# Performance work log

Hardware: AMD Instinct MI355X
Metric: run time of the kernel (lower is better)

Reference implementation:

```python
import jax, jax.numpy as jnp
import numpy as np

EPS = 1e-10
LN_EPS = 1e-5
NEG = -1e30
H = 8  # attention_head


def _layernorm(x, g, b):
    mu = jnp.mean(x, axis=-1, keepdims=True)
    var = jnp.mean(jnp.square(x - mu), axis=-1, keepdims=True)
    return (x - mu) * jax.lax.rsqrt(var + LN_EPS) * g + b


def setup_inputs() -> dict:
    key = jax.random.key(0)
    ks = jax.random.split(key, 10)
    B, T, D = 4, 1024, 1024
    inputs = jax.random.normal(ks[0], (B, T, D), dtype=jnp.float32)
    lengths = jax.random.randint(ks[1], (B,), T // 2, T + 1).astype(jnp.int32)
    lengths = lengths.at[0].set(T)  # at least one full-length sequence
    noise_u = jax.random.uniform(ks[2], (B, H, T, T), dtype=jnp.float32)
    w = lambda k: (jax.random.normal(k, (D, D), dtype=jnp.float32) * 0.02)
    return {
        'inputs': inputs, 'lengths': lengths, 'noise_u': noise_u,
        'Wq': w(ks[3]), 'Wk': w(ks[4]), 'Wv': w(ks[5]),
        'Weq': w(ks[6]), 'Wek': w(ks[7]), 'Wfc': w(ks[8]),
        'bfc': jnp.zeros((D,), jnp.float32),
        'ln1_g': jnp.ones((D,), jnp.float32), 'ln1_b': jnp.zeros((D,), jnp.float32),
        'ln2_g': jnp.ones((D,), jnp.float32), 'ln2_b': jnp.zeros((D,), jnp.float32),
    }


def reference(inputs, lengths, noise_u, Wq, Wk, Wv, Weq, Wek, Wfc, bfc,
              ln1_g, ln1_b, ln2_g, ln2_b):
    B, T, D = inputs.shape
    dh = D // H
    # length mask: True where padded
    pad = jnp.arange(T)[None, :] >= lengths[:, None]            # (B, T)
    x = jnp.where(pad[:, :, None], 0.0, inputs)                  # zero padded positions

    def heads(W):
        h = x @ W.T                                              # (B,T,D)
        return h.reshape(B, T, H, dh).transpose(0, 2, 1, 3)      # (B,H,T,dh)

    q, k, v, eq, ek = (heads(W) for W in (Wq, Wk, Wv, Weq, Wek))
    scores = jnp.einsum('bhqd,bhkd->bhqk', q, k) / jnp.sqrt(jnp.float32(D))
    edge = jnp.einsum('bhqd,bhkd->bhqk', eq, ek)                 # (B,H,T,T)

    # bernoulli prior: binary-concrete sample (hard threshold), tau=1
    edges_prob = jax.nn.sigmoid(edge)
    logistic = jnp.log(noise_u + EPS) - jnp.log(1.0 - noise_u + EPS)
    y_soft = jax.nn.sigmoid(jnp.log(edges_prob + EPS) - jnp.log(1.0 - edges_prob + EPS) + logistic)
    gate = y_soft > 0.5                                          # hard edges (condition only, as in torch .data)

    valid = gate & (~pad[:, None, None, :])                      # gate AND key-length mask
    s = jnp.where(valid, scores, NEG)
    attn = jax.nn.softmax(s, axis=-1)
    attn = jnp.where(jnp.any(valid, axis=-1, keepdims=True), attn, 0.0)  # nan->0 for fully-masked rows

    ctx = jax.nn.relu(jnp.einsum('bhqk,bhkd->bhqd', attn, v))
    ctx = ctx.transpose(0, 2, 1, 3).reshape(B, T, D)

    h1 = _layernorm(ctx + x, ln1_g, ln1_b)
    h2 = jax.nn.relu(h1 @ Wfc.T + bfc) + h1
    out = _layernorm(h2, ln2_g, ln2_b)
    out = jnp.where(pad[:, :, None], 0.0, out)
    return out, attn, edges_prob
```

## Files before the change

kernel.cpp:

```cpp
#include <hip/hip_runtime.h>
#include <math.h>

constexpr int Bn = 4, Tn = 1024, Dn = 1024, Hn = 8, DH = 128;
constexpr float EPSF = 1e-10f;
constexpr float LN_EPSF = 1e-5f;
constexpr float NEGF = -1e30f;

typedef __attribute__((ext_vector_type(8))) short bf16x8;
typedef __attribute__((ext_vector_type(4))) float f32x4;
typedef __attribute__((ext_vector_type(4))) unsigned uint4v;

#define MFMA16(a, b, c) __builtin_amdgcn_mfma_f32_16x16x32_bf16(a, b, c, 0, 0, 0)

__device__ __forceinline__ short f2bf(float f) {
    unsigned u = __builtin_bit_cast(unsigned, f);
    u += 0x7fffu + ((u >> 16) & 1u);
    return (short)(u >> 16);
}
__device__ __forceinline__ float bf2f(short h) {
    return __builtin_bit_cast(float, ((unsigned)(unsigned short)h) << 16);
}
__device__ __forceinline__ unsigned pack2(float a, float b) {
    return ((unsigned)(unsigned short)f2bf(a)) | (((unsigned)(unsigned short)f2bf(b)) << 16);
}

__device__ __forceinline__ void gload16(const void* g, void* l) {
    __builtin_amdgcn_global_load_lds((__attribute__((address_space(1))) void*)g,
                                     (__attribute__((address_space(3))) void*)l,
                                     16, 0, 0);
}

template <int NW>
__device__ __forceinline__ void stage_b(const short* g, int ld, short* lds, int lane, int wid) {
#pragma unroll
    for (int s = 0; s < 8 / NW; ++s) {
        const int ii = wid * (8 / NW) + s;
        const int c = ii * 64 + lane;
        const int kb = c >> 7, r = c & 127;
        gload16(g + (size_t)r * ld + kb * 8, lds + ii * 512);
    }
}

template <int NT>
__device__ __forceinline__ void stage64(const short* g, int ld, short* lds, int lane, int wid) {
    constexpr int IT = 1024 / NT;
#pragma unroll
    for (int s = 0; s < IT; ++s) {
        const int cb = wid * IT + s;
        const int c = cb * 64 + lane;
        const int kb = c >> 7, r = c & 127;
        gload16(g + (size_t)r * ld + kb * 8, lds + cb * 512);
    }
}

template <int NW>
__device__ __forceinline__ void stage_f(const float* g, int ld, float* lds, int lane, int wid) {
#pragma unroll
    for (int s = 0; s < 16 / NW; ++s) {
        const int ii = wid * (16 / NW) + s;
        const int c = ii * 64 + lane;
        const int kb = c >> 8, half = (c >> 7) & 1, r = c & 127;
        gload16(g + (size_t)r * ld + kb * 8 + half * 4, lds + ii * 256);
    }
}

__device__ __forceinline__ bf16x8 fragb(const short* lds, int kbl, int r) {
    return *reinterpret_cast<const bf16x8*>(lds + kbl * 1024 + r * 8);
}

__device__ __forceinline__ bf16x8 fragf(const float* lds, int kbl, int r) {
    const f32x4 lo = *reinterpret_cast<const f32x4*>(lds + kbl * 1024 + r * 4);
    const f32x4 hi = *reinterpret_cast<const f32x4*>(lds + kbl * 1024 + 512 + r * 4);
    uint4v p;
    p[0] = pack2(lo[0], lo[1]);
    p[1] = pack2(lo[2], lo[3]);
    p[2] = pack2(hi[0], hi[1]);
    p[3] = pack2(hi[2], hi[3]);
    return __builtin_bit_cast(bf16x8, p);
}

struct CvtP { const float* src[6]; short* hi; short* lo; };

__global__ __launch_bounds__(256) void cvt_w(CvtP p) {
    const int i = blockIdx.x * 256 + threadIdx.x;
    const int mat = i >> 17;
    const int off = (i & 131071) * 8;
    const float* s = p.src[mat] + off;
    const float4 a = *reinterpret_cast<const float4*>(s);
    const float4 b = *reinterpret_cast<const float4*>(s + 4);
    const float va[8] = {a.x, a.y, a.z, a.w, b.x, b.y, b.z, b.w};
    bf16x8 h, l;
#pragma unroll
    for (int j = 0; j < 8; ++j) {
        h[j] = f2bf(va[j]);
        l[j] = f2bf(va[j] - bf2f(h[j]));
    }
    *reinterpret_cast<bf16x8*>(p.hi + (size_t)mat * 1048576 + off) = h;
    if (mat == 3 || mat == 4)
        *reinterpret_cast<bf16x8*>(p.lo + (size_t)(mat - 3) * 1048576 + off) = l;
}

__global__ __launch_bounds__(256) void mask_x(const float4* __restrict__ in,
                                              const int* __restrict__ lengths,
                                              short* __restrict__ xhi,
                                              short* __restrict__ xlo) {
    const int i = blockIdx.x * 256 + threadIdx.x;
    const int row = i >> 8;
    const int t = row & 1023, b = row >> 10;
    float4 v = in[i];
    if (t >= lengths[b]) { v.x = 0.f; v.y = 0.f; v.z = 0.f; v.w = 0.f; }
    short4 h, l;
    h.x = f2bf(v.x); h.y = f2bf(v.y); h.z = f2bf(v.z); h.w = f2bf(v.w);
    l.x = f2bf(v.x - bf2f(h.x)); l.y = f2bf(v.y - bf2f(h.y));
    l.z = f2bf(v.z - bf2f(h.z)); l.w = f2bf(v.w - bf2f(h.w));
    *reinterpret_cast<short4*>(xhi + (size_t)i * 4) = h;
    *reinterpret_cast<short4*>(xlo + (size_t)i * 4) = l;
}

struct Proj3P { const short* w[3]; short* o[3]; };

__global__ __launch_bounds__(256) void proj3_mfma(const short* __restrict__ Xh, Proj3P p) {
    __shared__ alignas(16) short T0[8192];
    __shared__ alignas(16) short T1[8192];
    const int z = blockIdx.z;
    const short* __restrict__ Wh = p.w[z];
    const int m0 = blockIdx.y << 7, n0 = blockIdx.x << 7;
    const int tid = threadIdx.x, lane = tid & 63, wid = tid >> 6;
    const int wm = (wid >> 1) << 6, wn = (wid & 1) << 6;
    const int kbl = lane >> 4, rl = lane & 15, rw = (lane >> 4) << 2;
    f32x4 acc[4][4] = {};
    for (int k0 = 0; k0 < Dn; k0 += 64) {
        stage64<256>(Xh + (size_t)m0 * Dn + k0, Dn, T0, lane, wid);
        stage64<256>(Wh + (size_t)n0 * Dn + k0, Dn, T1, lane, wid);
        __syncthreads();
#pragma unroll
        for (int hh = 0; hh < 2; ++hh) {
            bf16x8 a[4], b[4];
#pragma unroll
            for (int f = 0; f < 4; ++f) {
                a[f] = fragb(T0, hh * 4 + kbl, wm + f * 16 + rl);
                b[f] = fragb(T1, hh * 4 + kbl, wn + f * 16 + rl);
            }
#pragma unroll
            for (int i = 0; i < 4; ++i)
#pragma unroll
                for (int j = 0; j < 4; ++j)
                    acc[i][j] = MFMA16(a[i], b[j], acc[i][j]);
        }
        __syncthreads();
    }
    short* __restrict__ O = p.o[z];
#pragma unroll
    for (int i = 0; i < 4; ++i)
#pragma unroll
        for (int r = 0; r < 4; ++r) {
            const int m = m0 + wm + i * 16 + rw + r;
            const int b = m >> 10, t = m & 1023;
#pragma unroll
            for (int j = 0; j < 4; ++j) {
                const int n = n0 + wn + j * 16 + rl;
                const int h = n >> 7, d = n & 127;
                const short val = f2bf(acc[i][j][r]);
                if (z == 2)
                    O[(((size_t)(b * Hn + h) * DH + d) << 10) + t] = val;
                else
                    O[((((size_t)(b * Hn + h)) << 10) + t) * DH + d] = val;
            }
        }
}

struct Proj2P { const short* wh[2]; const short* wl[2]; short* oh[2]; short* ol[2]; };

__global__ __launch_bounds__(512) void proj2_mfma(const short* __restrict__ Xh,
                                                  const short* __restrict__ Xl, Proj2P p) {
    __shared__ alignas(16) short T0[8192];
    __shared__ alignas(16) short T1[8192];
    __shared__ alignas(16) short T2[8192];
    __shared__ alignas(16) short T3[8192];
    const int z = blockIdx.z;
    const short* __restrict__ Wh = p.wh[z];
    const short* __restrict__ Wl = p.wl[z];
    const int m0 = blockIdx.y << 7, n0 = blockIdx.x << 7;
    const int tid = threadIdx.x, lane = tid & 63, wid = tid >> 6;
    const int wm = (wid >> 2) << 6, wn = (wid & 3) << 5;
    const int kbl = lane >> 4, rl = lane & 15, rw = (lane >> 4) << 2;
    f32x4 acc[4][2] = {};
    for (int k0 = 0; k0 < Dn; k0 += 64) {
        stage64<512>(Xh + (size_t)m0 * Dn + k0, Dn, T0, lane, wid);
        stage64<512>(Xl + (size_t)m0 * Dn + k0, Dn, T1, lane, wid);
        stage64<512>(Wh + (size_t)n0 * Dn + k0, Dn, T2, lane, wid);
        stage64<512>(Wl + (size_t)n0 * Dn + k0, Dn, T3, lane, wid);
        __syncthreads();
#pragma unroll
        for (int hh = 0; hh < 2; ++hh) {
            bf16x8 ah[4], al[4], bh[2], bl[2];
#pragma unroll
            for (int f = 0; f < 4; ++f) {
                ah[f] = fragb(T0, hh * 4 + kbl, wm + f * 16 + rl);
                al[f] = fragb(T1, hh * 4 + kbl, wm + f * 16 + rl);
            }
#pragma unroll
            for (int f = 0; f < 2; ++f) {
                bh[f] = fragb(T2, hh * 4 + kbl, wn + f * 16 + rl);
                bl[f] = fragb(T3, hh * 4 + kbl, wn + f * 16 + rl);
            }
#pragma unroll
            for (int i = 0; i < 4; ++i)
#pragma unroll
                for (int j = 0; j < 2; ++j) {
                    acc[i][j] = MFMA16(al[i], bh[j], acc[i][j]);
                    acc[i][j] = MFMA16(ah[i], bl[j], acc[i][j]);
                    acc[i][j] = MFMA16(ah[i], bh[j], acc[i][j]);
                }
        }
        __syncthreads();
    }
    short* __restrict__ OH = p.oh[z];
    short* __restrict__ OL = p.ol[z];
#pragma unroll
    for (int i = 0; i < 4; ++i)
#pragma unroll
        for (int r = 0; r < 4; ++r) {
            const int m = m0 + wm + i * 16 + rw + r;
            const int b = m >> 10, t = m & 1023;
#pragma unroll
            for (int j = 0; j < 2; ++j) {
                const int n = n0 + wn + j * 16 + rl;
                const int h = n >> 7, d = n & 127;
                const size_t idx = (((size_t)(b * Hn + h)) << 10 | t) * DH + d;
                const float av = acc[i][j][r];
                const short hi = f2bf(av);
                OH[idx] = hi;
                OL[idx] = f2bf(av - bf2f(hi));
            }
        }
}

__global__ __launch_bounds__(256) void scores_edge(
    const short* __restrict__ Q, const short* __restrict__ Kb,
    const short* __restrict__ EQh, const short* __restrict__ EQl,
    const short* __restrict__ EKh, const short* __restrict__ EKl,
    const float* __restrict__ U, const int* __restrict__ lens,
    float* __restrict__ S, float* __restrict__ EP,
    float* __restrict__ Sm, float* __restrict__ Sl) {
    __shared__ alignas(16) short T0[4096];
    __shared__ alignas(16) short T1[4096];
    __shared__ alignas(16) short T2[4096];
    __shared__ alignas(16) short T3[4096];
    const int z = blockIdx.z;
    const int len = lens[z >> 3];
    const int m0 = blockIdx.y << 7, n0 = blockIdx.x << 7;
    const int tid = threadIdx.x, lane = tid & 63, wid = tid >> 6;
    const int wm = (wid >> 1) << 6, wn = (wid & 1) << 6;
    const int kbl = lane >> 4, rl = lane & 15, rw = (lane >> 4) << 2;
    const size_t zo = (size_t)z << 17;

    f32x4 acce[4][4] = {};
    for (int k0 = 0; k0 < DH; k0 += 32) {
        stage_b<4>(EQh + zo + (size_t)m0 * DH + k0, DH, T0, lane, wid);
        stage_b<4>(EQl + zo + (size_t)m0 * DH + k0, DH, T1, lane, wid);
        stage_b<4>(EKh + zo + (size_t)n0 * DH + k0, DH, T2, lane, wid);
        stage_b<4>(EKl + zo + (size_t)n0 * DH + k0, DH, T3, lane, wid);
        __syncthreads();
        bf16x8 ah[4], al[4], bh[4], bl[4];
#pragma unroll
        for (int f = 0; f < 4; ++f) {
            ah[f] = fragb(T0, kbl, wm + f * 16 + rl);
            al[f] = fragb(T1, kbl, wm + f * 16 + rl);
            bh[f] = fragb(T2, kbl, wn + f * 16 + rl);
            bl[f] = fragb(T3, kbl, wn + f * 16 + rl);
        }
#pragma unroll
        for (int i = 0; i < 4; ++i)
#pragma unroll
            for (int j = 0; j < 4; ++j) {
                acce[i][j] = MFMA16(al[i], bh[j], acce[i][j]);
                acce[i][j] = MFMA16(ah[i], bl[j], acce[i][j]);
                acce[i][j] = MFMA16(ah[i], bh[j], acce[i][j]);
            }
        __syncthreads();
    }

    f32x4 accs[4][4] = {};
    for (int k0 = 0; k0 < DH; k0 += 32) {
        stage_b<4>(Q + zo + (size_t)m0 * DH + k0, DH, T0, lane, wid);
        stage_b<4>(Kb + zo + (size_t)n0 * DH + k0, DH, T1, lane, wid);
        __syncthreads();
        bf16x8 a[4], b[4];
#pragma unroll
        for (int f = 0; f < 4; ++f) {
            a[f] = fragb(T0, kbl, wm + f * 16 + rl);
            b[f] = fragb(T1, kbl, wn + f * 16 + rl);
        }
#pragma unroll
        for (int i = 0; i < 4; ++i)
#pragma unroll
            for (int j = 0; j < 4; ++j)
                accs[i][j] = MFMA16(a[i], b[j], accs[i][j]);
        __syncthreads();
    }

    const size_t part = ((size_t)(z * 16 + blockIdx.x * 2 + (wn >> 6)) << 10);
#pragma unroll
    for (int i = 0; i < 4; ++i)
#pragma unroll
        for (int r = 0; r < 4; ++r) {
            const int m = m0 + wm + i * 16 + rw + r;
            float sv[4];
#pragma unroll
            for (int j = 0; j < 4; ++j) {
                const int n = n0 + wn + j * 16 + rl;
                const size_t idx = ((size_t)z << 20) + ((size_t)m << 10) + n;
                const float e = acce[i][j][r];
                EP[idx] = 1.f / (1.f + __expf(-e));
                const float u = U[idx];
                const float zz = e + __logf(u + EPSF) - __logf(1.f - u + EPSF);
                const bool valid = (zz > 0.f) && (n < len);
                const float s_val = valid ? accs[i][j][r] * (1.f / 32.f) : NEGF;
                S[idx] = s_val;
                sv[j] = s_val;
            }
            float mx = fmaxf(fmaxf(sv[0], sv[1]), fmaxf(sv[2], sv[3]));
#pragma unroll
            for (int off = 1; off <= 8; off <<= 1) mx = fmaxf(mx, __shfl_xor(mx, off));
            float ls = __expf(sv[0] - mx) + __expf(sv[1] - mx) +
                       __expf(sv[2] - mx) + __expf(sv[3] - mx);
#pragma unroll
            for (int off = 1; off <= 8; off <<= 1) ls += __shfl_xor(ls, off);
            if (rl == 0) { Sm[part + m] = mx; Sl[part + m] = ls; }
        }
}

__global__ __launch_bounds__(512) void softmax_ctx(float* __restrict__ P,
                                                   const float* __restrict__ Sm,
                                                   const float* __restrict__ Sl,
                                                   const short* __restrict__ Vt,
                                                   float* __restrict__ C) {
    __shared__ alignas(16) float Ps[4096];
    __shared__ alignas(16) short Vs[4096];
    const int z = blockIdx.y;
    const int bb = z >> 3, h = z & 7;
    const int m0 = blockIdx.x << 7;
    const int tid = threadIdx.x, lane = tid & 63, wid = tid >> 6;

    {
        const int r = tid >> 2, qd = tid & 3;
        const int row = m0 + r;
        float M = -3.0e38f;
#pragma unroll
        for (int t = 0; t < 16; ++t) M = fmaxf(M, Sm[((size_t)(z * 16 + t) << 10) + row]);
        float L = 0.f;
#pragma unroll
        for (int t = 0; t < 16; ++t)
            L += Sl[((size_t)(z * 16 + t) << 10) + row] *
                 __expf(Sm[((size_t)(z * 16 + t) << 10) + row] - M);
        const float inv = (M > -5e29f) ? 1.f / L : 0.f;
        float* rowp = P + ((size_t)z << 20) + ((size_t)row << 10) + qd * 8;
#pragma unroll 8
        for (int c = 0; c < 32; ++c) {
            float4 v0 = *reinterpret_cast<const float4*>(rowp + c * 32);
            float4 v1 = *reinterpret_cast<const float4*>(rowp + c * 32 + 4);
            v0.x = __expf(v0.x - M) * inv; v0.y = __expf(v0.y - M) * inv;
            v0.z = __expf(v0.z - M) * inv; v0.w = __expf(v0.w - M) * inv;
            v1.x = __expf(v1.x - M) * inv; v1.y = __expf(v1.y - M) * inv;
            v1.z = __expf(v1.z - M) * inv; v1.w = __expf(v1.w - M) * inv;
            *reinterpret_cast<float4*>(rowp + c * 32) = v0;
            *reinterpret_cast<float4*>(rowp + c * 32 + 4) = v1;
        }
    }
    __syncthreads();

    const int wm = (wid >> 2) << 6, wn = (wid & 3) << 5;
    const int kbl = lane >> 4, rl = lane & 15, rw = (lane >> 4) << 2;
    f32x4 acc[4][2] = {};
    for (int k0 = 0; k0 < Tn; k0 += 32) {
        stage_f<8>(P + ((size_t)z << 20) + ((size_t)m0 << 10) + k0, Tn, Ps, lane, wid);
        stage_b<8>(Vt + ((size_t)z << 17) + k0, Tn, Vs, lane, wid);
        __syncthreads();
        bf16x8 a[4], b[2];
#pragma unroll
        for (int f = 0; f < 4; ++f) a[f] = fragf(Ps, kbl, wm + f * 16 + rl);
#pragma unroll
        for (int f = 0; f < 2; ++f) b[f] = fragb(Vs, kbl, wn + f * 16 + rl);
#pragma unroll
        for (int i = 0; i < 4; ++i)
#pragma unroll
            for (int j = 0; j < 2; ++j)
                acc[i][j] = MFMA16(a[i], b[j], acc[i][j]);
        __syncthreads();
    }
#pragma unroll
    for (int i = 0; i < 4; ++i)
#pragma unroll
        for (int r = 0; r < 4; ++r) {
            const int m = m0 + wm + i * 16 + rw + r;
#pragma unroll
            for (int j = 0; j < 2; ++j) {
                const int n = wn + j * 16 + rl;
                C[(((size_t)(bb << 10 | m)) << 10) + h * DH + n] = fmaxf(acc[i][j][r], 0.f);
            }
        }
}

__global__ __launch_bounds__(256) void ln1_kernel(const float* __restrict__ ctx,
                                                  const float* __restrict__ inputs,
                                                  const int* __restrict__ lengths,
                                                  const float* __restrict__ g,
                                                  const float* __restrict__ bb,
                                                  float* __restrict__ h1f,
                                                  short* __restrict__ h1hi) {
    __shared__ float red1[4];
    __shared__ float red2[4];
    const int row = blockIdx.x;
    const int t = row & 1023, b = row >> 10;
    const bool live = t < lengths[b];
    const size_t base = (size_t)row * Dn;
    const int tid = threadIdx.x;
    float4 v = reinterpret_cast<const float4*>(ctx + base)[tid];
    if (live) {
        const float4 r = reinterpret_cast<const float4*>(inputs + base)[tid];
        v.x += r.x; v.y += r.y; v.z += r.z; v.w += r.w;
    }
    float s = v.x + v.y + v.z + v.w;
#pragma unroll
    for (int off = 32; off >= 1; off >>= 1) s += __shfl_xor(s, off);
    if ((tid & 63) == 0) red1[tid >> 6] = s;
    __syncthreads();
    const float mu = (red1[0] + red1[1] + red1[2] + red1[3]) * (1.f / Dn);
    const float d0 = v.x - mu, d1 = v.y - mu, d2 = v.z - mu, d3 = v.w - mu;
    float sq = d0 * d0 + d1 * d1 + d2 * d2 + d3 * d3;
#pragma unroll
    for (int off = 32; off >= 1; off >>= 1) sq += __shfl_xor(sq, off);
    if ((tid & 63) == 0) red2[tid >> 6] = sq;
    __syncthreads();
    const float var = (red2[0] + red2[1] + red2[2] + red2[3]) * (1.f / Dn);
    const float rstd = rsqrtf(var + LN_EPSF);
    const float4 gv = reinterpret_cast<const float4*>(g)[tid];
    const float4 bv = reinterpret_cast<const float4*>(bb)[tid];
    float4 ov;
    ov.x = d0 * rstd * gv.x + bv.x;
    ov.y = d1 * rstd * gv.y + bv.y;
    ov.z = d2 * rstd * gv.z + bv.z;
    ov.w = d3 * rstd * gv.w + bv.w;
    reinterpret_cast<float4*>(h1f + base)[tid] = ov;
    short4 hs;
    hs.x = f2bf(ov.x); hs.y = f2bf(ov.y); hs.z = f2bf(ov.z); hs.w = f2bf(ov.w);
    reinterpret_cast<short4*>(h1hi + base)[tid] = hs;
}

__global__ __launch_bounds__(256) void fc_mfma(const short* __restrict__ Xh,
                                               const short* __restrict__ Wh,
                                               const float* __restrict__ bias,
                                               const float* __restrict__ H1f,
                                               float* __restrict__ O) {
    __shared__ alignas(16) short T0[8192];
    __shared__ alignas(16) short T1[8192];
    const int m0 = blockIdx.y << 7, n0 = blockIdx.x << 7;
    const int tid = threadIdx.x, lane = tid & 63, wid = tid >> 6;
    const int wm = (wid >> 1) << 6, wn = (wid & 1) << 6;
    const int kbl = lane >> 4, rl = lane & 15, rw = (lane >> 4) << 2;
    f32x4 acc[4][4] = {};
    for (int k0 = 0; k0 < Dn; k0 += 64) {
        stage64<256>(Xh + (size_t)m0 * Dn + k0, Dn, T0, lane, wid);
        stage64<256>(Wh + (size_t)n0 * Dn + k0, Dn, T1, lane, wid);
        __syncthreads();
#pragma unroll
        for (int hh = 0; hh < 2; ++hh) {
            bf16x8 a[4], b[4];
#pragma unroll
            for (int f = 0; f < 4; ++f) {
                a[f] = fragb(T0, hh * 4 + kbl, wm + f * 16 + rl);
                b[f] = fragb(T1, hh * 4 + kbl, wn + f * 16 + rl);
            }
#pragma unroll
            for (int i = 0; i < 4; ++i)
#pragma unroll
                for (int j = 0; j < 4; ++j)
                    acc[i][j] = MFMA16(a[i], b[j], acc[i][j]);
        }
        __syncthreads();
    }
#pragma unroll
    for (int i = 0; i < 4; ++i)
#pragma unroll
        for (int r = 0; r < 4; ++r) {
            const int m = m0 + wm + i * 16 + rw + r;
#pragma unroll
            for (int j = 0; j < 4; ++j) {
                const int n = n0 + wn + j * 16 + rl;
                const size_t idx = ((size_t)m << 10) + n;
                O[idx] = fmaxf(acc[i][j][r] + bias[n], 0.f) + H1f[idx];
            }
        }
}

__global__ __launch_bounds__(256) void ln2_kernel(const float* __restrict__ a,
                                                  const float* __restrict__ g,
                                                  const float* __restrict__ bb,
                                                  const int* __restrict__ lengths,
                                                  float* __restrict__ o) {
    __shared__ float red1[4];
    __shared__ float red2[4];
    const int row = blockIdx.x;
    const size_t base = (size_t)row * Dn;
    const int tid = threadIdx.x;
    float4 v = reinterpret_cast<const float4*>(a + base)[tid];
    float s = v.x + v.y + v.z + v.w;
#pragma unroll
    for (int off = 32; off >= 1; off >>= 1) s += __shfl_xor(s, off);
    if ((tid & 63) == 0) red1[tid >> 6] = s;
    __syncthreads();
    const float mu = (red1[0] + red1[1] + red1[2] + red1[3]) * (1.f / Dn);
    const float d0 = v.x - mu, d1 = v.y - mu, d2 = v.z - mu, d3 = v.w - mu;
    float sq = d0 * d0 + d1 * d1 + d2 * d2 + d3 * d3;
#pragma unroll
    for (int off = 32; off >= 1; off >>= 1) sq += __shfl_xor(sq, off);
    if ((tid & 63) == 0) red2[tid >> 6] = sq;
    __syncthreads();
    const float var = (red2[0] + red2[1] + red2[2] + red2[3]) * (1.f / Dn);
    const float rstd = rsqrtf(var + LN_EPSF);
    const float4 gv = reinterpret_cast<const float4*>(g)[tid];
    const float4 bv = reinterpret_cast<const float4*>(bb)[tid];
    float4 ov;
    ov.x = d0 * rstd * gv.x + bv.x;
    ov.y = d1 * rstd * gv.y + bv.y;
    ov.z = d2 * rstd * gv.z + bv.z;
    ov.w = d3 * rstd * gv.w + bv.w;
    const int t = row & 1023, b = row >> 10;
    if (t >= lengths[b]) { ov.x = 0.f; ov.y = 0.f; ov.z = 0.f; ov.w = 0.f; }
    reinterpret_cast<float4*>(o + base)[tid] = ov;
}

extern "C" void kernel_launch(void* const* d_in, const int* in_sizes, int n_in,
                              void* d_out, int out_size, void* d_ws, size_t ws_size,
                              hipStream_t stream) {
    const float* inputs = (const float*)d_in[0];
    const int* lengths = (const int*)d_in[1];
    const float* noise = (const float*)d_in[2];
    const float* bfc = (const float*)d_in[9];
    const float* ln1_g = (const float*)d_in[10];
    const float* ln1_b = (const float*)d_in[11];
    const float* ln2_g = (const float*)d_in[12];
    const float* ln2_b = (const float*)d_in[13];

    float* out = (float*)d_out;
    float* attn = out + (size_t)Bn * Tn * Dn;
    float* ep = attn + (size_t)Bn * Hn * Tn * Tn;

    constexpr size_t MB = 1u << 20;
    char* W = (char*)d_ws;
    short* xhi = (short*)(W + 0 * MB);
    short* xlo = (short*)(W + 8 * MB);
    short* whi = (short*)(W + 16 * MB);
    short* wlo = (short*)(W + 28 * MB);
    short* qb = (short*)(W + 34 * MB);
    short* kb = (short*)(W + 42 * MB);
    short* vtb = (short*)(W + 50 * MB);
    short* eqh = (short*)(W + 58 * MB);
    short* eql = (short*)(W + 66 * MB);
    short* ekh = (short*)(W + 74 * MB);
    short* ekl = (short*)(W + 82 * MB);
    float* ctx = (float*)(W + 58 * MB);
    float* h1f = (float*)(W + 74 * MB);
    short* h1hi = (short*)(W + 34 * MB);
    float* h2 = (float*)(W + 0 * MB);
    float* Sm = (float*)(W + 90 * MB);
    float* Sl = (float*)(W + 92 * MB);

    CvtP cp;
    for (int j = 0; j < 6; ++j) cp.src[j] = (const float*)d_in[3 + j];
    cp.hi = whi; cp.lo = wlo;
    cvt_w<<<dim3(3072), 256, 0, stream>>>(cp);

    mask_x<<<dim3(4096), 256, 0, stream>>>((const float4*)inputs, lengths, xhi, xlo);

    Proj3P p3;
    p3.w[0] = whi;                 p3.o[0] = qb;
    p3.w[1] = whi + 1 * 1048576;   p3.o[1] = kb;
    p3.w[2] = whi + 2 * 1048576;   p3.o[2] = vtb;
    proj3_mfma<<<dim3(8, 32, 3), 256, 0, stream>>>(xhi, p3);

    Proj2P p2;
    p2.wh[0] = whi + 3 * 1048576;  p2.wl[0] = wlo;
    p2.wh[1] = whi + 4 * 1048576;  p2.wl[1] = wlo + 1048576;
    p2.oh[0] = eqh; p2.ol[0] = eql;
    p2.oh[1] = ekh; p2.ol[1] = ekl;
    proj2_mfma<<<dim3(8, 32, 2), 512, 0, stream>>>(xhi, xlo, p2);

    scores_edge<<<dim3(8, 8, 32), 256, 0, stream>>>(qb, kb, eqh, eql, ekh, ekl,
                                                    noise, lengths, attn, ep, Sm, Sl);

    softmax_ctx<<<dim3(8, 32), 512, 0, stream>>>(attn, Sm, Sl, vtb, ctx);

    ln1_kernel<<<dim3(Bn * Tn), 256, 0, stream>>>(ctx, inputs, lengths, ln1_g, ln1_b,
                                                  h1f, h1hi);

    fc_mfma<<<dim3(8, 32), 256, 0, stream>>>(h1hi, whi + 5 * 1048576, bfc, h1f, h2);

    ln2_kernel<<<dim3(Bn * Tn), 256, 0, stream>>>(h2, ln2_g, ln2_b, lengths, out);
}
```

Baseline: 500.2 us.

## Drop softmax max-subtraction and simplify gate test to p+u>1

Scores are stored as unnormalized exp(s/32) values, with masked entries set to zero, so the per-tile row max array and the rescaling pass are removed. The softmax kernel only sums the partial row sums and multiplies by the inverse, with no second exp. The binary-concrete gate is reduced algebraically from two logs to the comparison sigmoid(e)+u>1. This relies on the score magnitudes being small enough that exp does not overflow without a max shift, and the gate rewrite drops the EPS terms, so decisions can differ near the threshold.

```diff
diff --git a/kernel.cpp b/kernel.cpp
--- a/kernel.cpp
+++ b/kernel.cpp
@@ -2,9 +2,7 @@
 #include <math.h>
 
 constexpr int Bn = 4, Tn = 1024, Dn = 1024, Hn = 8, DH = 128;
-constexpr float EPSF = 1e-10f;
 constexpr float LN_EPSF = 1e-5f;
-constexpr float NEGF = -1e30f;
 
 typedef __attribute__((ext_vector_type(8))) short bf16x8;
 typedef __attribute__((ext_vector_type(4))) float f32x4;
@@ -242,7 +240,7 @@
     const short* __restrict__ EKh, const short* __restrict__ EKl,
     const float* __restrict__ U, const int* __restrict__ lens,
     float* __restrict__ S, float* __restrict__ EP,
-    float* __restrict__ Sm, float* __restrict__ Sl) {
+    float* __restrict__ Sl) {
     __shared__ alignas(16) short T0[4096];
     __shared__ alignas(16) short T1[4096];
     __shared__ alignas(16) short T2[4096];
@@ -306,33 +304,28 @@
 #pragma unroll
         for (int r = 0; r < 4; ++r) {
             const int m = m0 + wm + i * 16 + rw + r;
-            float sv[4];
+            float ev[4];
 #pragma unroll
             for (int j = 0; j < 4; ++j) {
                 const int n = n0 + wn + j * 16 + rl;
                 const size_t idx = ((size_t)z << 20) + ((size_t)m << 10) + n;
                 const float e = acce[i][j][r];
-                EP[idx] = 1.f / (1.f + __expf(-e));
+                const float pp = 1.f / (1.f + __expf(-e));
+                EP[idx] = pp;
                 const float u = U[idx];
-                const float zz = e + __logf(u + EPSF) - __logf(1.f - u + EPSF);
-                const bool valid = (zz > 0.f) && (n < len);
-                const float s_val = valid ? accs[i][j][r] * (1.f / 32.f) : NEGF;
-                S[idx] = s_val;
-                sv[j] = s_val;
-            }
-            float mx = fmaxf(fmaxf(sv[0], sv[1]), fmaxf(sv[2], sv[3]));
-#pragma unroll
-            for (int off = 1; off <= 8; off <<= 1) mx = fmaxf(mx, __shfl_xor(mx, off));
-            float ls = __expf(sv[0] - mx) + __expf(sv[1] - mx) +
-                       __expf(sv[2] - mx) + __expf(sv[3] - mx);
+                const bool valid = (pp + u > 1.f) && (n < len);
+                const float E = valid ? __expf(accs[i][j][r] * (1.f / 32.f)) : 0.f;
+                S[idx] = E;
+                ev[j] = E;
+            }
+            float ls = ev[0] + ev[1] + ev[2] + ev[3];
 #pragma unroll
             for (int off = 1; off <= 8; off <<= 1) ls += __shfl_xor(ls, off);
-            if (rl == 0) { Sm[part + m] = mx; Sl[part + m] = ls; }
+            if (rl == 0) Sl[part + m] = ls;
         }
 }
 
 __global__ __launch_bounds__(512) void softmax_ctx(float* __restrict__ P,
-                                                   const float* __restrict__ Sm,
                                                    const float* __restrict__ Sl,
                                                    const short* __restrict__ Vt,
                                                    float* __restrict__ C) {
@@ -346,24 +339,17 @@
     {
         const int r = tid >> 2, qd = tid & 3;
         const int row = m0 + r;
-        float M = -3.0e38f;
-#pragma unroll
-        for (int t = 0; t < 16; ++t) M = fmaxf(M, Sm[((size_t)(z * 16 + t) << 10) + row]);
         float L = 0.f;
 #pragma unroll
-        for (int t = 0; t < 16; ++t)
-            L += Sl[((size_t)(z * 16 + t) << 10) + row] *
-                 __expf(Sm[((size_t)(z * 16 + t) << 10) + row] - M);
-        const float inv = (M > -5e29f) ? 1.f / L : 0.f;
+        for (int t = 0; t < 16; ++t) L += Sl[((size_t)(z * 16 + t) << 10) + row];
+        const float inv = (L > 0.f) ? 1.f / L : 0.f;
         float* rowp = P + ((size_t)z << 20) + ((size_t)row << 10) + qd * 8;
 #pragma unroll 8
         for (int c = 0; c < 32; ++c) {
             float4 v0 = *reinterpret_cast<const float4*>(rowp + c * 32);
             float4 v1 = *reinterpret_cast<const float4*>(rowp + c * 32 + 4);
-            v0.x = __expf(v0.x - M) * inv; v0.y = __expf(v0.y - M) * inv;
-            v0.z = __expf(v0.z - M) * inv; v0.w = __expf(v0.w - M) * inv;
-            v1.x = __expf(v1.x - M) * inv; v1.y = __expf(v1.y - M) * inv;
-            v1.z = __expf(v1.z - M) * inv; v1.w = __expf(v1.w - M) * inv;
+            v0.x *= inv; v0.y *= inv; v0.z *= inv; v0.w *= inv;
+            v1.x *= inv; v1.y *= inv; v1.z *= inv; v1.w *= inv;
             *reinterpret_cast<float4*>(rowp + c * 32) = v0;
             *reinterpret_cast<float4*>(rowp + c * 32 + 4) = v1;
         }
@@ -564,8 +550,7 @@
     float* h1f = (float*)(W + 74 * MB);
     short* h1hi = (short*)(W + 34 * MB);
     float* h2 = (float*)(W + 0 * MB);
-    float* Sm = (float*)(W + 90 * MB);
-    float* Sl = (float*)(W + 92 * MB);
+    float* Sl = (float*)(W + 90 * MB);
 
     CvtP cp;
     for (int j = 0; j < 6; ++j) cp.src[j] = (const float*)d_in[3 + j];
@@ -588,9 +573,9 @@
     proj2_mfma<<<dim3(8, 32, 2), 512, 0, stream>>>(xhi, xlo, p2);
 
     scores_edge<<<dim3(8, 8, 32), 256, 0, stream>>>(qb, kb, eqh, eql, ekh, ekl,
-                                                    noise, lengths, attn, ep, Sm, Sl);
-
-    softmax_ctx<<<dim3(8, 32), 512, 0, stream>>>(attn, Sm, Sl, vtb, ctx);
+                                                    noise, lengths, attn, ep, Sl);
+
+    softmax_ctx<<<dim3(8, 32), 512, 0, stream>>>(attn, Sl, vtb, ctx);
 
     ln1_kernel<<<dim3(Bn * Tn), 256, 0, stream>>>(ctx, inputs, lengths, ln1_g, ln1_b,
                                                   h1f, h1hi);
```

Measured after the change: 610.0 us. 1.22x slower.
